# Optimization experiments

Measured on AMD Instinct MI355X. Metric: run time of the kernel, lower is better.

Reference implementation:

```python
import jax, jax.numpy as jnp
import numpy as np

B, C, DET, T = 16, 1, 512, 180  # batch, channels, detector size (= image side, circle=True), n angles


def setup_inputs() -> dict:
    key = jax.random.key(0)
    x = jax.random.normal(key, (B, C, DET, T), dtype=jnp.float32)  # sinogram [B,C,det,theta]
    return {"x": x}


def _ramp_filter(x):
    """skimage-style ramp (Ram-Lak) filter along detector axis (axis=2)."""
    det = x.shape[2]
    size = max(64, int(2 ** np.ceil(np.log2(2 * det))))  # zero-padded FFT length
    n = np.concatenate([np.arange(1, size // 2 + 1, 2), np.arange(size // 2 - 1, 0, -2)])
    f = np.zeros(size, dtype=np.float64)
    f[0] = 0.25
    f[1::2] = -1.0 / (np.pi * n) ** 2
    fourier = (2.0 * np.real(np.fft.fft(f))).astype(np.float32)  # [size]
    xp = jnp.pad(x, ((0, 0), (0, 0), (0, size - det), (0, 0)))
    proj = jnp.fft.fft(xp, axis=2) * fourier[None, None, :, None]
    return jnp.real(jnp.fft.ifft(proj, axis=2))[:, :, :det, :].astype(x.dtype)


def _forward(x):
    b, c, det, n_theta = x.shape
    xf = _ramp_filter(x)
    # align_corners=False unit grid over the image (circle=True -> grid side == det)
    u = ((2.0 * jnp.arange(det, dtype=x.dtype) + 1.0) / det - 1.0)
    yg = u[:, None]  # [det,1] (meshgrid 'ij': Y varies over rows)
    xg = u[None, :]  # [1,det]
    rad = jnp.arange(n_theta, dtype=x.dtype) * jnp.asarray(np.pi / 180.0, x.dtype)
    cos_t, sin_t = jnp.cos(rad), jnp.sin(rad)

    # Note: the grid X coord theta_x[i]=(2i+1)/T-1 maps (align_corners=False) to pixel
    # index exactly i, so the width-axis bilinear interp reduces to taking angle column i.
    def body(reco, inp):
        i, c_, s_ = inp
        col = jax.lax.dynamic_index_in_dim(xf, i, axis=3, keepdims=False)  # [B,C,det]
        t = xg * c_ - yg * s_                      # [det,det] rotated coordinate
        iy = ((t + 1.0) * det - 1.0) / 2.0         # grid_sample align_corners=False
        i0f = jnp.floor(iy)
        w1 = iy - i0f
        w0 = 1.0 - w1
        i0 = i0f.astype(jnp.int32)
        i1 = i0 + 1
        m0 = ((i0 >= 0) & (i0 < det)).astype(xf.dtype)  # zeros padding
        m1 = ((i1 >= 0) & (i1 < det)).astype(xf.dtype)
        g0 = jnp.take(col, jnp.clip(i0, 0, det - 1), axis=2)  # [B,C,det,det]
        g1 = jnp.take(col, jnp.clip(i1, 0, det - 1), axis=2)
        return reco + (w0 * m0) * g0 + (w1 * m1) * g1, None

    reco0 = jnp.zeros((b, c, det, det), xf.dtype)
    reco, _ = jax.lax.scan(body, reco0, (jnp.arange(n_theta), cos_t, sin_t))

    # reconstruction circle mask (scikit=False -> radius^2 <= 1 - 1/in_size)
    mask = (xg ** 2 + yg ** 2) <= (1.0 - 1.0 / det)
    reco = jnp.where(mask[None, None], reco, jnp.zeros((), reco.dtype))
    return reco * jnp.asarray(np.pi / (2.0 * n_theta), reco.dtype)


def reference(x):
    return _forward(x)
```

## Files before the change

kernel.cpp:

```cpp
#include <hip/hip_runtime.h>
#include <math.h>

#define DET 512
#define NB  16
#define NT  180
#define PI_D 3.14159265358979323846
#define NPAIR 89
#define PADQ 108
#define NGP  45
#define PKI_ROW 1536
#define NUNIT 113

#define TT_OFF   8192
#define XF0_OFF  (TT_OFF + 512*512*2)
#define XF90_OFF (XF0_OFF + 32768)
#define PK_OFF   (XF90_OFF + 32768)

typedef _Float16 half8  __attribute__((ext_vector_type(8)));
typedef _Float16 half4v __attribute__((ext_vector_type(4)));
typedef _Float16 half2v __attribute__((ext_vector_type(2)));
typedef float    float4v __attribute__((ext_vector_type(4)));

__device__ inline void fmix_lo(float& acc, float w, unsigned int pk) {
  asm("v_fma_mix_f32 %0, %1, %2, %0 op_sel_hi:[0,1,0]"
      : "+v"(acc) : "v"(w), "v"(pk));
}
__device__ inline void fmix_hi(float& acc, float w, unsigned int pk) {
  asm("v_fma_mix_f32 %0, %1, %2, %0 op_sel:[0,1,0] op_sel_hi:[0,1,0]"
      : "+v"(acc) : "v"(w), "v"(pk));
}

__global__ __launch_bounds__(256) void filter_kernel(const float* __restrict__ x,
                                                     char* __restrict__ wsb) {
  __shared__ _Float16 xs_h[16][512];
  __shared__ _Float16 xs_l[16][512];
  __shared__ float xfs[16][65];
  __shared__ _Float16 wls[8][1032];
  unsigned int* pkg = (unsigned int*)(wsb + PK_OFF);

  int tid = threadIdx.x;
  int p = blockIdx.x, b = blockIdx.y;
  int dt0 = blockIdx.z * 2;

  {
    int k0 = tid * 4;
    const float CSC = (float)(-2048.0 / (PI_D * PI_D));
#pragma unroll
    for (int r = 0; r < 8; r++) {
      half4v v;
#pragma unroll
      for (int j = 0; j < 4; j++) {
        int delta = 511 - (k0 + j) - r;
        float wv;
        if (delta == 0) wv = 512.0f;
        else if (delta & 1) wv = CSC / (float)(delta * delta);
        else wv = 0.0f;
        v[j] = (_Float16)wv;
      }
      *(half4v*)&wls[r][k0] = v;
    }
  }

  int m = tid & 15, kp = tid >> 4;
  int tS;
  if (p < 11) tS = (m < 8) ? (8 * p + 1 + m) : (164 - 8 * p + m);
  else        tS = (m == 0) ? 89 : ((m == 1) ? 91 : ((m == 3) ? 90 : 0));
  const float* xb = x + (size_t)b * DET * NT + tS;
#pragma unroll 8
  for (int pass = 0; pass < 16; pass++) {
    int k = pass * 32 + kp * 2;
    int c = k >> 3, h = k & 7;
    int phys = (((c ^ (m & 7)) << 3) | h);
    float v0 = xb[(size_t)k * NT];
    float v1 = xb[(size_t)(k + 1) * NT];
    _Float16 h0 = (_Float16)v0, h1 = (_Float16)v1;
    half2v hh = {h0, h1};
    half2v ll = {(_Float16)(v0 - (float)h0), (_Float16)(v1 - (float)h1)};
    *(half2v*)&xs_h[m][phys] = hh;
    *(half2v*)&xs_l[m][phys] = ll;
  }
  __syncthreads();

  int nprb = (p < 11) ? 8 : 1;
  int tpb0 = (p < 11) ? 8 * p : 88;
  if (blockIdx.z == 0) {
    int idx = (tid < 108) ? tid : (620 + (tid - 108));
    uint2 z2; z2.x = 0u; z2.y = 0u;
    for (int pr = 0; pr < nprb; pr++) {
      int tq = (p < 11) ? (tpb0 + pr) : 88;
      int gp = (tq <= 44) ? tq : 88 - tq;
      *(uint2*)&pkg[((size_t)b * NGP + gp) * PKI_ROW + 2 * idx] = z2;
    }
  }

  int lane = tid & 63, wv = tid >> 6;
  int mm = lane & 15, q = lane >> 4;
  const _Float16* arh = &xs_h[mm][0];
  const _Float16* arl = &xs_l[mm][0];
  int e = mm & 7;
  int mp = tid >> 5, cc = (tid & 31) * 2;
  int rT = (p < 11) ? mp : 0;
  int rU = (p < 11) ? (15 - mp) : 1;
  int tpp = (p < 11) ? (8 * p + mp) : 88;
  bool dopack = (p < 11) || (mp == 0);
  int gp_  = (tpp <= 44) ? tpp : 88 - tpp;
  int slot = (tpp <= 44) ? 0 : 1;

  for (int dti = 0; dti < 2; dti++) {
    int dt = dt0 + dti;
    int dw = dt * 64 + wv * 16 + mm;
    int sdw = 511 - dw;
    const _Float16* thl = &wls[sdw & 7][sdw & ~7];
    float4v acc0 = {0.f, 0.f, 0.f, 0.f};
    float4v acc1 = {0.f, 0.f, 0.f, 0.f};
#pragma unroll 4
    for (int kc = 0; kc < 512; kc += 32) {
      int ph = ((((kc >> 3) + q) ^ e) << 3);
      half8 Ah = *(const half8*)&arh[ph];
      half8 Al = *(const half8*)&arl[ph];
      half8 Bh = *(const half8*)&thl[kc + q * 8];
      acc0 = __builtin_amdgcn_mfma_f32_16x16x32_f16(Ah, Bh, acc0, 0, 0, 0);
      acc1 = __builtin_amdgcn_mfma_f32_16x16x32_f16(Al, Bh, acc1, 0, 0, 0);
    }
    if (dti > 0) __syncthreads();
#pragma unroll
    for (int i = 0; i < 4; i++)
      xfs[q * 4 + i][wv * 16 + mm] = (acc0[i] + acc1[i]) * 0.0009765625f;
    __syncthreads();
    if (dopack) {
      float ft0 = xfs[rT][cc], ft1 = xfs[rT][cc + 1];
      float fu0 = xfs[rU][cc], fu1 = xfs[rU][cc + 1];
      auto p0 = __builtin_amdgcn_cvt_pkrtz(ft0, fu0);
      auto p1 = __builtin_amdgcn_cvt_pkrtz(ft1, fu1);
      unsigned int w0, w1;
      __builtin_memcpy(&w0, &p0, 4);
      __builtin_memcpy(&w1, &p1, 4);
      unsigned int* row = pkg + ((size_t)b * NGP + gp_) * PKI_ROW;
      int en = PADQ + dt * 64 + cc;
      row[2 * en + slot]     = w0;
      row[2 * en + 2 + slot] = w1;
      if (tpp == 44) {
        row[2 * en + 1] = w0;
        row[2 * en + 3] = w1;
      }
    }
    if (p == 11 && tid < 64) {
      float* f0  = (float*)(wsb + XF0_OFF)  + (size_t)b * DET;
      float* f90 = (float*)(wsb + XF90_OFF) + (size_t)b * DET;
      f0[dt * 64 + tid]  = xfs[2][tid];
      f90[dt * 64 + tid] = xfs[3][tid];
    }
  }
}

#define PROCESS(c_, s_, SW)                                                    \
  {                                                                            \
    float inner = fmaf(-(s_), q_, 363.5f);                                     \
    float iyA = fmaf( (c_), p_, inner);                                        \
    float iyB = fmaf(-(c_), p_, inner);                                        \
    int   iA = (int)iyA;  float wA = __builtin_amdgcn_fractf(iyA);             \
    int   iB = (int)iyB;  float wB = __builtin_amdgcn_fractf(iyB);             \
    float vA = 1.f - wA, vB = 1.f - wB;                                        \
    uint4 rA, rB, rMA, rMB;                                                    \
    __builtin_memcpy(&rA,  &colI[2 * iA], 16);                                 \
    __builtin_memcpy(&rB,  &colI[2 * iB], 16);                                 \
    __builtin_memcpy(&rMA, &colI[2 * (726 - iA)], 16);                         \
    __builtin_memcpy(&rMB, &colI[2 * (726 - iB)], 16);                         \
    unsigned tA0 = SW ? rA.y : rA.x,  tA1 = SW ? rA.w : rA.z;                  \
    unsigned uA0 = SW ? rA.x : rA.y,  uA1 = SW ? rA.z : rA.w;                  \
    unsigned tB0 = SW ? rB.y : rB.x,  tB1 = SW ? rB.w : rB.z;                  \
    unsigned uB0 = SW ? rB.x : rB.y,  uB1 = SW ? rB.z : rB.w;                  \
    unsigned tMA0 = SW ? rMA.y : rMA.x,  tMA1 = SW ? rMA.w : rMA.z;            \
    unsigned uMA0 = SW ? rMA.x : rMA.y,  uMA1 = SW ? rMA.z : rMA.w;            \
    unsigned tMB0 = SW ? rMB.y : rMB.x,  tMB1 = SW ? rMB.w : rMB.z;            \
    unsigned uMB0 = SW ? rMB.x : rMB.y,  uMB1 = SW ? rMB.z : rMB.w;            \
    fmix_lo(A1, vA, tA0);  fmix_lo(A1, wA, tA1);                               \
    fmix_hi(A1, vB, tB0);  fmix_hi(A1, wB, tB1);                               \
    fmix_lo(A2, vB, tB0);  fmix_lo(A2, wB, tB1);                               \
    fmix_hi(A2, vA, tA0);  fmix_hi(A2, wA, tA1);                               \
    fmix_lo(A3, wA, tMA0); fmix_lo(A3, vA, tMA1);                              \
    fmix_hi(A3, wB, tMB0); fmix_hi(A3, vB, tMB1);                              \
    fmix_lo(A4, wB, tMB0); fmix_lo(A4, vB, tMB1);                              \
    fmix_hi(A4, wA, tMA0); fmix_hi(A4, vA, tMA1);                              \
    if (doQ) {                                                                 \
      fmix_lo(B1, wA, uMA0); fmix_lo(B1, vA, uMA1);                            \
      fmix_hi(B1, vB, uB0);  fmix_hi(B1, wB, uB1);                             \
      fmix_lo(B2, wB, uMB0); fmix_lo(B2, vB, uMB1);                            \
      fmix_hi(B2, vA, uA0);  fmix_hi(B2, wA, uA1);                             \
      fmix_lo(B3, vA, uA0);  fmix_lo(B3, wA, uA1);                             \
      fmix_hi(B3, wB, uMB0); fmix_hi(B3, vB, uMB1);                            \
      fmix_lo(B4, vB, uB0);  fmix_lo(B4, wB, uB1);                             \
      fmix_hi(B4, wA, uMA0); fmix_hi(B4, vA, uMA1);                            \
    }                                                                          \
  }

__global__ __launch_bounds__(256, 8) void backproj_kernel(
    const char* __restrict__ wsb, float* __restrict__ out) {
  __shared__ unsigned int pk[2][PKI_ROW];
  __shared__ float2 trigs[48];
  int tid = threadIdx.x;
  int b   = blockIdx.y;
  int bx  = blockIdx.x;
  int lx = tid & 15, ly = tid >> 4;
  float* ob = out + (size_t)b * DET * DET;

  if (bx == NUNIT) {
    const int LDEAD[10] = {10,8,6,5,4,3,2,2,1,1};
    for (int a = 0; a < 10; a++)
      for (int bt = 0; bt < LDEAD[a]; bt++) {
        int X1 = 16*a + lx, X2 = 511 - X1;
        int Y1 = 16*bt + ly, Y2 = 511 - Y1;
        ob[(size_t)Y1*DET + X1] = 0.f;
        ob[(size_t)Y1*DET + X2] = 0.f;
        ob[(size_t)Y2*DET + X1] = 0.f;
        ob[(size_t)Y2*DET + X2] = 0.f;
      }
    return;
  }

  int a = (bx>=6)+(bx>=14)+(bx>=24)+(bx>=35)+(bx>=47)+(bx>=58)+(bx>=68)
        + (bx>=77)+(bx>=85)+(bx>=92)+(bx>=98)+(bx>=103)+(bx>=107)+(bx>=110)+(bx>=112);
  int Sa, bs;
  if (a < 8) { Sa = (int)((0x443A2F23180E0600ULL >> (8*a)) & 0xFF);
               bs = (int)((0x070605040506080AULL >> (8*a)) & 0xFF); }
  else       { Sa = (int)((0x706E6B67625C554DULL >> (8*(a-8))) & 0xFF);
               bs = (int)((0x0F0E0D0C0B0A0908ULL >> (8*(a-8))) & 0xFF); }
  int bt = bx - Sa + bs;
  bool doQ = (a != bt);
  int tx = 16*a, ty = 16*bt;

  int X1 = tx + lx, X2 = 511 - X1;
  int Y1 = ty + ly, Y2 = 511 - Y1;
  float p_ = (float)X1 - 255.5f;
  float q_ = (float)Y1 - 255.5f;

  int w = tid >> 6, l = tid & 63;
  int mkx = 481 - 32*a;
  int mky = 505 - 32*bt - 8*w;
  bool wlive = (mkx*mkx + mky*mky <= 261632);

  if (tid < NGP) {
    float th = (float)(tid + 1) * (float)(PI_D / 180.0);
    float2 cs; cs.x = cosf(th); cs.y = sinf(th);
    trigs[tid] = cs;
  }

  const unsigned int* pkg = (const unsigned int*)(wsb + PK_OFF) + (size_t)b * NGP * PKI_ROW;

  float A1=0.f, A2=0.f, A3=0.f, A4=0.f;
  float B1=0.f, B2=0.f, B3=0.f, B4=0.f;

  auto stage_group = [&](int g, int par) {
    {
      const unsigned int* src = pkg + (size_t)g * PKI_ROW + w * 256 + l * 4;
      char* dst = (char*)&pk[par][0] + w * 1024;
      __builtin_amdgcn_global_load_lds(
          (const __attribute__((address_space(1))) unsigned int*)src,
          (__attribute__((address_space(3))) unsigned int*)dst, 16, 0, 0);
    }
    if (w < 2) {
      const unsigned int* src = pkg + (size_t)g * PKI_ROW + (w + 4) * 256 + l * 4;
      char* dst = (char*)&pk[par][0] + (w + 4) * 1024;
      __builtin_amdgcn_global_load_lds(
          (const __attribute__((address_space(1))) unsigned int*)src,
          (__attribute__((address_space(3))) unsigned int*)dst, 16, 0, 0);
    }
  };

  stage_group(0, 0);
  __syncthreads();

  for (int g = 0; g < NGP; g++) {
    if (g + 1 < NGP) stage_group(g + 1, (g + 1) & 1);
    float2 cs = trigs[g];
    const unsigned int* colI = &pk[g & 1][0];
    if (wlive) {
      PROCESS(cs.x, cs.y, 0);
      if (g != 44) PROCESS(cs.y, cs.x, 1);
    }
    __syncthreads();
  }

  const float* f0  = (const float*)(wsb + XF0_OFF)  + (size_t)b * DET;
  const float* f90 = (const float*)(wsb + XF90_OFF) + (size_t)b * DET;
  const float SC = (float)(PI_D / 360.0);
  int kx = 2*X1 - 511, ky = 2*Y1 - 511;
  bool in = (kx*kx + ky*ky) <= 261632;

  float g0x1 = f0[X1], g0x2 = f0[X2];
  float g90y1 = f90[Y1], g90y2 = f90[Y2];
  float P1 = A1 + g0x1 + g90y2;
  float P2 = A2 + g0x2 + g90y2;
  float P3 = A3 + g0x2 + g90y1;
  float P4 = A4 + g0x1 + g90y1;
  ob[(size_t)Y1*DET + X1] = in ? P1*SC : 0.f;
  ob[(size_t)Y1*DET + X2] = in ? P2*SC : 0.f;
  ob[(size_t)Y2*DET + X2] = in ? P3*SC : 0.f;
  ob[(size_t)Y2*DET + X1] = in ? P4*SC : 0.f;

  if (doQ) {
    float g0y1 = f0[Y1], g0y2 = f0[Y2];
    float g90x1 = f90[X1], g90x2 = f90[X2];
    float Q1 = B1 + g0y1 + g90x2;
    float Q2 = B2 + g0y1 + g90x1;
    float Q3 = B3 + g0y2 + g90x1;
    float Q4 = B4 + g0y2 + g90x2;
    Q1 = in ? Q1*SC : 0.f;
    Q2 = in ? Q2*SC : 0.f;
    Q3 = in ? Q3*SC : 0.f;
    Q4 = in ? Q4*SC : 0.f;
    __syncthreads();
    float* qs = (float*)&pk[0][0];
    qs[(0*16 + lx)*17 + ly] = Q1;
    qs[(1*16 + lx)*17 + ly] = Q2;
    qs[(2*16 + lx)*17 + ly] = Q3;
    qs[(3*16 + lx)*17 + ly] = Q4;
    __syncthreads();
    float o1 = qs[(0*16 + ly)*17 + lx];
    float o2 = qs[(1*16 + ly)*17 + lx];
    float o3 = qs[(2*16 + ly)*17 + lx];
    float o4 = qs[(3*16 + ly)*17 + lx];
    int r1 = tx + ly, r2 = 511 - r1;
    int c1 = ty + lx, c2 = 511 - c1;
    ob[(size_t)r1*DET + c1] = o1;
    ob[(size_t)r2*DET + c1] = o2;
    ob[(size_t)r2*DET + c2] = o3;
    ob[(size_t)r1*DET + c2] = o4;
  }
}

extern "C" void kernel_launch(void* const* d_in, const int* in_sizes, int n_in,
                              void* d_out, int out_size, void* d_ws, size_t ws_size,
                              hipStream_t stream) {
  (void)in_sizes; (void)n_in; (void)out_size; (void)ws_size;
  const float* x = (const float*)d_in[0];
  float* out = (float*)d_out;
  char*  wsb = (char*)d_ws;

  filter_kernel<<<dim3(12, 16, 4), 256, 0, stream>>>(x, wsb);
  backproj_kernel<<<dim3(NUNIT + 1, 16), 256, 0, stream>>>(wsb, out);
}
```

Before: 142.1 us.

## Process two batch images per backprojection block to share coordinate math

Each backprojection block now handles two batch items. The per-pixel interpolation coordinates and weights are computed once and reused for both images' LDS columns. LDS staging, accumulators and output writes are doubled, the grid's batch dimension is halved, and launch bounds drop to 4 blocks/SM. This amortizes the index/weight arithmetic and trig setup, at the cost of more registers and LDS per block, fewer blocks (less parallelism), and lower occupancy.

```diff
diff --git a/kernel.cpp b/kernel.cpp
--- a/kernel.cpp
+++ b/kernel.cpp
@@ -153,6 +153,41 @@
   }
 }
 
+#define RDFMIX(colX, rr, SW)                                                   \
+  {                                                                            \
+    uint4 rA, rB, rMA, rMB;                                                    \
+    __builtin_memcpy(&rA,  &colX[2 * iA], 16);                                 \
+    __builtin_memcpy(&rB,  &colX[2 * iB], 16);                                 \
+    __builtin_memcpy(&rMA, &colX[2 * (726 - iA)], 16);                         \
+    __builtin_memcpy(&rMB, &colX[2 * (726 - iB)], 16);                         \
+    unsigned tA0 = SW ? rA.y : rA.x,  tA1 = SW ? rA.w : rA.z;                  \
+    unsigned uA0 = SW ? rA.x : rA.y,  uA1 = SW ? rA.z : rA.w;                  \
+    unsigned tB0 = SW ? rB.y : rB.x,  tB1 = SW ? rB.w : rB.z;                  \
+    unsigned uB0 = SW ? rB.x : rB.y,  uB1 = SW ? rB.z : rB.w;                  \
+    unsigned tMA0 = SW ? rMA.y : rMA.x,  tMA1 = SW ? rMA.w : rMA.z;            \
+    unsigned uMA0 = SW ? rMA.x : rMA.y,  uMA1 = SW ? rMA.z : rMA.w;            \
+    unsigned tMB0 = SW ? rMB.y : rMB.x,  tMB1 = SW ? rMB.w : rMB.z;            \
+    unsigned uMB0 = SW ? rMB.x : rMB.y,  uMB1 = SW ? rMB.z : rMB.w;            \
+    fmix_lo(A1[rr], vA, tA0);  fmix_lo(A1[rr], wA, tA1);                       \
+    fmix_hi(A1[rr], vB, tB0);  fmix_hi(A1[rr], wB, tB1);                       \
+    fmix_lo(A2[rr], vB, tB0);  fmix_lo(A2[rr], wB, tB1);                       \
+    fmix_hi(A2[rr], vA, tA0);  fmix_hi(A2[rr], wA, tA1);                       \
+    fmix_lo(A3[rr], wA, tMA0); fmix_lo(A3[rr], vA, tMA1);                      \
+    fmix_hi(A3[rr], wB, tMB0); fmix_hi(A3[rr], vB, tMB1);                      \
+    fmix_lo(A4[rr], wB, tMB0); fmix_lo(A4[rr], vB, tMB1);                      \
+    fmix_hi(A4[rr], wA, tMA0); fmix_hi(A4[rr], vA, tMA1);                      \
+    if (doQ) {                                                                 \
+      fmix_lo(B1[rr], wA, uMA0); fmix_lo(B1[rr], vA, uMA1);                    \
+      fmix_hi(B1[rr], vB, uB0);  fmix_hi(B1[rr], wB, uB1);                     \
+      fmix_lo(B2[rr], wB, uMB0); fmix_lo(B2[rr], vB, uMB1);                    \
+      fmix_hi(B2[rr], vA, uA0);  fmix_hi(B2[rr], wA, uA1);                     \
+      fmix_lo(B3[rr], vA, uA0);  fmix_lo(B3[rr], wA, uA1);                     \
+      fmix_hi(B3[rr], wB, uMB0); fmix_hi(B3[rr], vB, uMB1);                    \
+      fmix_lo(B4[rr], vB, uB0);  fmix_lo(B4[rr], wB, uB1);                     \
+      fmix_hi(B4[rr], wA, uMA0); fmix_hi(B4[rr], vA, uMA1);                    \
+    }                                                                          \
+  }
+
 #define PROCESS(c_, s_, SW)                                                    \
   {                                                                            \
     float inner = fmaf(-(s_), q_, 363.5f);                                     \
@@ -161,48 +196,20 @@
     int   iA = (int)iyA;  float wA = __builtin_amdgcn_fractf(iyA);             \
     int   iB = (int)iyB;  float wB = __builtin_amdgcn_fractf(iyB);             \
     float vA = 1.f - wA, vB = 1.f - wB;                                        \
-    uint4 rA, rB, rMA, rMB;                                                    \
-    __builtin_memcpy(&rA,  &colI[2 * iA], 16);                                 \
-    __builtin_memcpy(&rB,  &colI[2 * iB], 16);                                 \
-    __builtin_memcpy(&rMA, &colI[2 * (726 - iA)], 16);                         \
-    __builtin_memcpy(&rMB, &colI[2 * (726 - iB)], 16);                         \
-    unsigned tA0 = SW ? rA.y : rA.x,  tA1 = SW ? rA.w : rA.z;                  \
-    unsigned uA0 = SW ? rA.x : rA.y,  uA1 = SW ? rA.z : rA.w;                  \
-    unsigned tB0 = SW ? rB.y : rB.x,  tB1 = SW ? rB.w : rB.z;                  \
-    unsigned uB0 = SW ? rB.x : rB.y,  uB1 = SW ? rB.z : rB.w;                  \
-    unsigned tMA0 = SW ? rMA.y : rMA.x,  tMA1 = SW ? rMA.w : rMA.z;            \
-    unsigned uMA0 = SW ? rMA.x : rMA.y,  uMA1 = SW ? rMA.z : rMA.w;            \
-    unsigned tMB0 = SW ? rMB.y : rMB.x,  tMB1 = SW ? rMB.w : rMB.z;            \
-    unsigned uMB0 = SW ? rMB.x : rMB.y,  uMB1 = SW ? rMB.z : rMB.w;            \
-    fmix_lo(A1, vA, tA0);  fmix_lo(A1, wA, tA1);                               \
-    fmix_hi(A1, vB, tB0);  fmix_hi(A1, wB, tB1);                               \
-    fmix_lo(A2, vB, tB0);  fmix_lo(A2, wB, tB1);                               \
-    fmix_hi(A2, vA, tA0);  fmix_hi(A2, wA, tA1);                               \
-    fmix_lo(A3, wA, tMA0); fmix_lo(A3, vA, tMA1);                              \
-    fmix_hi(A3, wB, tMB0); fmix_hi(A3, vB, tMB1);                              \
-    fmix_lo(A4, wB, tMB0); fmix_lo(A4, vB, tMB1);                              \
-    fmix_hi(A4, wA, tMA0); fmix_hi(A4, vA, tMA1);                              \
-    if (doQ) {                                                                 \
-      fmix_lo(B1, wA, uMA0); fmix_lo(B1, vA, uMA1);                            \
-      fmix_hi(B1, vB, uB0);  fmix_hi(B1, wB, uB1);                             \
-      fmix_lo(B2, wB, uMB0); fmix_lo(B2, vB, uMB1);                            \
-      fmix_hi(B2, vA, uA0);  fmix_hi(B2, wA, uA1);                             \
-      fmix_lo(B3, vA, uA0);  fmix_lo(B3, wA, uA1);                             \
-      fmix_hi(B3, wB, uMB0); fmix_hi(B3, vB, uMB1);                            \
-      fmix_lo(B4, vB, uB0);  fmix_lo(B4, wB, uB1);                             \
-      fmix_hi(B4, wA, uMA0); fmix_hi(B4, vA, uMA1);                            \
-    }                                                                          \
-  }
-
-__global__ __launch_bounds__(256, 8) void backproj_kernel(
+    RDFMIX(colI0, 0, SW)                                                       \
+    RDFMIX(colI1, 1, SW)                                                       \
+  }
+
+__global__ __launch_bounds__(256, 4) void backproj_kernel(
     const char* __restrict__ wsb, float* __restrict__ out) {
-  __shared__ unsigned int pk[2][PKI_ROW];
+  __shared__ unsigned int pk[2][2][PKI_ROW];
   __shared__ float2 trigs[48];
   int tid = threadIdx.x;
-  int b   = blockIdx.y;
+  int b0  = blockIdx.y * 2;
   int bx  = blockIdx.x;
   int lx = tid & 15, ly = tid >> 4;
-  float* ob = out + (size_t)b * DET * DET;
+  float* ob0 = out + (size_t)b0 * DET * DET;
+  float* ob1 = out + (size_t)(b0 + 1) * DET * DET;
 
   if (bx == NUNIT) {
     const int LDEAD[10] = {10,8,6,5,4,3,2,2,1,1};
@@ -210,10 +217,10 @@
       for (int bt = 0; bt < LDEAD[a]; bt++) {
         int X1 = 16*a + lx, X2 = 511 - X1;
         int Y1 = 16*bt + ly, Y2 = 511 - Y1;
-        ob[(size_t)Y1*DET + X1] = 0.f;
-        ob[(size_t)Y1*DET + X2] = 0.f;
-        ob[(size_t)Y2*DET + X1] = 0.f;
-        ob[(size_t)Y2*DET + X2] = 0.f;
+        ob0[(size_t)Y1*DET + X1] = 0.f;  ob1[(size_t)Y1*DET + X1] = 0.f;
+        ob0[(size_t)Y1*DET + X2] = 0.f;  ob1[(size_t)Y1*DET + X2] = 0.f;
+        ob0[(size_t)Y2*DET + X1] = 0.f;  ob1[(size_t)Y2*DET + X1] = 0.f;
+        ob0[(size_t)Y2*DET + X2] = 0.f;  ob1[(size_t)Y2*DET + X2] = 0.f;
       }
     return;
   }
@@ -245,26 +252,24 @@
     trigs[tid] = cs;
   }
 
-  const unsigned int* pkg = (const unsigned int*)(wsb + PK_OFF) + (size_t)b * NGP * PKI_ROW;
-
-  float A1=0.f, A2=0.f, A3=0.f, A4=0.f;
-  float B1=0.f, B2=0.f, B3=0.f, B4=0.f;
+  const unsigned int* pkg0 = (const unsigned int*)(wsb + PK_OFF) + (size_t)b0 * NGP * PKI_ROW;
+  const unsigned int* pkg1 = pkg0 + (size_t)NGP * PKI_ROW;
+
+  float A1[2]={0,0}, A2[2]={0,0}, A3[2]={0,0}, A4[2]={0,0};
+  float B1[2]={0,0}, B2[2]={0,0}, B3[2]={0,0}, B4[2]={0,0};
 
   auto stage_group = [&](int g, int par) {
-    {
-      const unsigned int* src = pkg + (size_t)g * PKI_ROW + w * 256 + l * 4;
-      char* dst = (char*)&pk[par][0] + w * 1024;
+#pragma unroll
+    for (int i = 0; i < 3; i++) {
+      int c = w + 4 * i;
+      int r = (c < 6) ? 0 : 1;
+      int off = (c < 6) ? c : (c - 6);
+      const unsigned int* src = (r ? pkg1 : pkg0) + (size_t)g * PKI_ROW + off * 256 + l * 4;
+      char* dst = (char*)&pk[par][r][0] + off * 1024;
       __builtin_amdgcn_global_load_lds(
           (const __attribute__((address_space(1))) unsigned int*)src,
           (__attribute__((address_space(3))) unsigned int*)dst, 16, 0, 0);
     }
-    if (w < 2) {
-      const unsigned int* src = pkg + (size_t)g * PKI_ROW + (w + 4) * 256 + l * 4;
-      char* dst = (char*)&pk[par][0] + (w + 4) * 1024;
-      __builtin_amdgcn_global_load_lds(
-          (const __attribute__((address_space(1))) unsigned int*)src,
-          (__attribute__((address_space(3))) unsigned int*)dst, 16, 0, 0);
-    }
   };
 
   stage_group(0, 0);
@@ -273,7 +278,8 @@
   for (int g = 0; g < NGP; g++) {
     if (g + 1 < NGP) stage_group(g + 1, (g + 1) & 1);
     float2 cs = trigs[g];
-    const unsigned int* colI = &pk[g & 1][0];
+    const unsigned int* colI0 = &pk[g & 1][0][0];
+    const unsigned int* colI1 = &pk[g & 1][1][0];
     if (wlive) {
       PROCESS(cs.x, cs.y, 0);
       if (g != 44) PROCESS(cs.y, cs.x, 1);
@@ -281,51 +287,61 @@
     __syncthreads();
   }
 
-  const float* f0  = (const float*)(wsb + XF0_OFF)  + (size_t)b * DET;
-  const float* f90 = (const float*)(wsb + XF90_OFF) + (size_t)b * DET;
   const float SC = (float)(PI_D / 360.0);
   int kx = 2*X1 - 511, ky = 2*Y1 - 511;
   bool in = (kx*kx + ky*ky) <= 261632;
 
-  float g0x1 = f0[X1], g0x2 = f0[X2];
-  float g90y1 = f90[Y1], g90y2 = f90[Y2];
-  float P1 = A1 + g0x1 + g90y2;
-  float P2 = A2 + g0x2 + g90y2;
-  float P3 = A3 + g0x2 + g90y1;
-  float P4 = A4 + g0x1 + g90y1;
-  ob[(size_t)Y1*DET + X1] = in ? P1*SC : 0.f;
-  ob[(size_t)Y1*DET + X2] = in ? P2*SC : 0.f;
-  ob[(size_t)Y2*DET + X2] = in ? P3*SC : 0.f;
-  ob[(size_t)Y2*DET + X1] = in ? P4*SC : 0.f;
+  float Qs[2][4];
+#pragma unroll
+  for (int rr = 0; rr < 2; rr++) {
+    const float* f0  = (const float*)(wsb + XF0_OFF)  + (size_t)(b0 + rr) * DET;
+    const float* f90 = (const float*)(wsb + XF90_OFF) + (size_t)(b0 + rr) * DET;
+    float* ob = rr ? ob1 : ob0;
+    float g0x1 = f0[X1], g0x2 = f0[X2];
+    float g90y1 = f90[Y1], g90y2 = f90[Y2];
+    float P1 = A1[rr] + g0x1 + g90y2;
+    float P2 = A2[rr] + g0x2 + g90y2;
+    float P3 = A3[rr] + g0x2 + g90y1;
+    float P4 = A4[rr] + g0x1 + g90y1;
+    ob[(size_t)Y1*DET + X1] = in ? P1*SC : 0.f;
+    ob[(size_t)Y1*DET + X2] = in ? P2*SC : 0.f;
+    ob[(size_t)Y2*DET + X2] = in ? P3*SC : 0.f;
+    ob[(size_t)Y2*DET + X1] = in ? P4*SC : 0.f;
+    if (doQ) {
+      float g0y1 = f0[Y1], g0y2 = f0[Y2];
+      float g90x1 = f90[X1], g90x2 = f90[X2];
+      Qs[rr][0] = in ? (B1[rr] + g0y1 + g90x2) * SC : 0.f;
+      Qs[rr][1] = in ? (B2[rr] + g0y1 + g90x1) * SC : 0.f;
+      Qs[rr][2] = in ? (B3[rr] + g0y2 + g90x1) * SC : 0.f;
+      Qs[rr][3] = in ? (B4[rr] + g0y2 + g90x2) * SC : 0.f;
+    }
+  }
 
   if (doQ) {
-    float g0y1 = f0[Y1], g0y2 = f0[Y2];
-    float g90x1 = f90[X1], g90x2 = f90[X2];
-    float Q1 = B1 + g0y1 + g90x2;
-    float Q2 = B2 + g0y1 + g90x1;
-    float Q3 = B3 + g0y2 + g90x1;
-    float Q4 = B4 + g0y2 + g90x2;
-    Q1 = in ? Q1*SC : 0.f;
-    Q2 = in ? Q2*SC : 0.f;
-    Q3 = in ? Q3*SC : 0.f;
-    Q4 = in ? Q4*SC : 0.f;
     __syncthreads();
-    float* qs = (float*)&pk[0][0];
-    qs[(0*16 + lx)*17 + ly] = Q1;
-    qs[(1*16 + lx)*17 + ly] = Q2;
-    qs[(2*16 + lx)*17 + ly] = Q3;
-    qs[(3*16 + lx)*17 + ly] = Q4;
+    float* qs0 = (float*)&pk[0][0][0];
+    float* qs1 = (float*)&pk[0][1][0];
+#pragma unroll
+    for (int i = 0; i < 4; i++) {
+      qs0[(i*16 + lx)*17 + ly] = Qs[0][i];
+      qs1[(i*16 + lx)*17 + ly] = Qs[1][i];
+    }
     __syncthreads();
-    float o1 = qs[(0*16 + ly)*17 + lx];
-    float o2 = qs[(1*16 + ly)*17 + lx];
-    float o3 = qs[(2*16 + ly)*17 + lx];
-    float o4 = qs[(3*16 + ly)*17 + lx];
     int r1 = tx + ly, r2 = 511 - r1;
     int c1 = ty + lx, c2 = 511 - c1;
-    ob[(size_t)r1*DET + c1] = o1;
-    ob[(size_t)r2*DET + c1] = o2;
-    ob[(size_t)r2*DET + c2] = o3;
-    ob[(size_t)r1*DET + c2] = o4;
+#pragma unroll
+    for (int rr = 0; rr < 2; rr++) {
+      float* qs = rr ? qs1 : qs0;
+      float* ob = rr ? ob1 : ob0;
+      float o1 = qs[(0*16 + ly)*17 + lx];
+      float o2 = qs[(1*16 + ly)*17 + lx];
+      float o3 = qs[(2*16 + ly)*17 + lx];
+      float o4 = qs[(3*16 + ly)*17 + lx];
+      ob[(size_t)r1*DET + c1] = o1;
+      ob[(size_t)r2*DET + c1] = o2;
+      ob[(size_t)r2*DET + c2] = o3;
+      ob[(size_t)r1*DET + c2] = o4;
+    }
   }
 }
 
@@ -338,5 +354,5 @@
   char*  wsb = (char*)d_ws;
 
   filter_kernel<<<dim3(12, 16, 4), 256, 0, stream>>>(x, wsb);
-  backproj_kernel<<<dim3(NUNIT + 1, 16), 256, 0, stream>>>(wsb, out);
-}
+  backproj_kernel<<<dim3(NUNIT + 1, NB / 2), 256, 0, stream>>>(wsb, out);
+}
```

New measurement: 145.4 us. +2.4%, slower.

## Merge diagonal tile pairs into single blocks and drop doQ branch from off-diagonal path

Applied to the files above, without the earlier changes.

Diagonal tiles (a==bt), which only computed the P half of the symmetric work, are now paired two per block in a dedicated path that processes two diagonal tiles sharing the same staged LDS columns. Off-diagonal blocks always do the Q work, so the per-angle doQ branch disappears, and the grid shrinks from 114 to 108 blocks per batch. The aim is better load balance, since diagonal blocks no longer run half-empty, and fewer redundant staging passes. The cost is a more complex index mapping and a second specialised code path, which can raise register pressure.

```diff
diff --git a/kernel.cpp b/kernel.cpp
--- a/kernel.cpp
+++ b/kernel.cpp
@@ -9,7 +9,9 @@
 #define PADQ 108
 #define NGP  45
 #define PKI_ROW 1536
-#define NUNIT 113
+#define NOFF 101
+#define NMRG 6
+#define NBX  108
 
 #define TT_OFF   8192
 #define XF0_OFF  (TT_OFF + 512*512*2)
@@ -152,6 +154,7 @@
     }
   }
 }
+
 
 #define PROCESS(c_, s_, SW)                                                    \
   {                                                                            \
@@ -182,16 +185,41 @@
     fmix_hi(A3, wB, tMB0); fmix_hi(A3, vB, tMB1);                              \
     fmix_lo(A4, wB, tMB0); fmix_lo(A4, vB, tMB1);                              \
     fmix_hi(A4, wA, tMA0); fmix_hi(A4, vA, tMA1);                              \
-    if (doQ) {                                                                 \
-      fmix_lo(B1, wA, uMA0); fmix_lo(B1, vA, uMA1);                            \
-      fmix_hi(B1, vB, uB0);  fmix_hi(B1, wB, uB1);                             \
-      fmix_lo(B2, wB, uMB0); fmix_lo(B2, vB, uMB1);                            \
-      fmix_hi(B2, vA, uA0);  fmix_hi(B2, wA, uA1);                             \
-      fmix_lo(B3, vA, uA0);  fmix_lo(B3, wA, uA1);                             \
-      fmix_hi(B3, wB, uMB0); fmix_hi(B3, vB, uMB1);                            \
-      fmix_lo(B4, vB, uB0);  fmix_lo(B4, wB, uB1);                             \
-      fmix_hi(B4, wA, uMA0); fmix_hi(B4, vA, uMA1);                            \
-    }                                                                          \
+    fmix_lo(B1, wA, uMA0); fmix_lo(B1, vA, uMA1);                              \
+    fmix_hi(B1, vB, uB0);  fmix_hi(B1, wB, uB1);                               \
+    fmix_lo(B2, wB, uMB0); fmix_lo(B2, vB, uMB1);                              \
+    fmix_hi(B2, vA, uA0);  fmix_hi(B2, wA, uA1);                               \
+    fmix_lo(B3, vA, uA0);  fmix_lo(B3, wA, uA1);                               \
+    fmix_hi(B3, wB, uMB0); fmix_hi(B3, vB, uMB1);                              \
+    fmix_lo(B4, vB, uB0);  fmix_lo(B4, wB, uB1);                               \
+    fmix_hi(B4, wA, uMA0); fmix_hi(B4, vA, uMA1);                              \
+  }
+
+#define PROCESSP(c_, s_, SW, pp, qq, AA1, AA2, AA3, AA4)                       \
+  {                                                                            \
+    float inner = fmaf(-(s_), (qq), 363.5f);                                   \
+    float iyA = fmaf( (c_), (pp), inner);                                      \
+    float iyB = fmaf(-(c_), (pp), inner);                                      \
+    int   iA = (int)iyA;  float wA = __builtin_amdgcn_fractf(iyA);             \
+    int   iB = (int)iyB;  float wB = __builtin_amdgcn_fractf(iyB);             \
+    float vA = 1.f - wA, vB = 1.f - wB;                                        \
+    uint4 rA, rB, rMA, rMB;                                                    \
+    __builtin_memcpy(&rA,  &colI[2 * iA], 16);                                 \
+    __builtin_memcpy(&rB,  &colI[2 * iB], 16);                                 \
+    __builtin_memcpy(&rMA, &colI[2 * (726 - iA)], 16);                         \
+    __builtin_memcpy(&rMB, &colI[2 * (726 - iB)], 16);                         \
+    unsigned tA0 = SW ? rA.y : rA.x,  tA1 = SW ? rA.w : rA.z;                  \
+    unsigned tB0 = SW ? rB.y : rB.x,  tB1 = SW ? rB.w : rB.z;                  \
+    unsigned tMA0 = SW ? rMA.y : rMA.x,  tMA1 = SW ? rMA.w : rMA.z;            \
+    unsigned tMB0 = SW ? rMB.y : rMB.x,  tMB1 = SW ? rMB.w : rMB.z;            \
+    fmix_lo(AA1, vA, tA0);  fmix_lo(AA1, wA, tA1);                             \
+    fmix_hi(AA1, vB, tB0);  fmix_hi(AA1, wB, tB1);                             \
+    fmix_lo(AA2, vB, tB0);  fmix_lo(AA2, wB, tB1);                             \
+    fmix_hi(AA2, vA, tA0);  fmix_hi(AA2, wA, tA1);                             \
+    fmix_lo(AA3, wA, tMA0); fmix_lo(AA3, vA, tMA1);                            \
+    fmix_hi(AA3, wB, tMB0); fmix_hi(AA3, vB, tMB1);                            \
+    fmix_lo(AA4, wB, tMB0); fmix_lo(AA4, vB, tMB1);                            \
+    fmix_hi(AA4, wA, tMA0); fmix_hi(AA4, vA, tMA1);                            \
   }
 
 __global__ __launch_bounds__(256, 8) void backproj_kernel(
@@ -203,8 +231,9 @@
   int bx  = blockIdx.x;
   int lx = tid & 15, ly = tid >> 4;
   float* ob = out + (size_t)b * DET * DET;
-
-  if (bx == NUNIT) {
+  int w = tid >> 6, l = tid & 63;
+
+  if (bx == NOFF + NMRG) {
     const int LDEAD[10] = {10,8,6,5,4,3,2,2,1,1};
     for (int a = 0; a < 10; a++)
       for (int bt = 0; bt < LDEAD[a]; bt++) {
@@ -218,27 +247,6 @@
     return;
   }
 
-  int a = (bx>=6)+(bx>=14)+(bx>=24)+(bx>=35)+(bx>=47)+(bx>=58)+(bx>=68)
-        + (bx>=77)+(bx>=85)+(bx>=92)+(bx>=98)+(bx>=103)+(bx>=107)+(bx>=110)+(bx>=112);
-  int Sa, bs;
-  if (a < 8) { Sa = (int)((0x443A2F23180E0600ULL >> (8*a)) & 0xFF);
-               bs = (int)((0x070605040506080AULL >> (8*a)) & 0xFF); }
-  else       { Sa = (int)((0x706E6B67625C554DULL >> (8*(a-8))) & 0xFF);
-               bs = (int)((0x0F0E0D0C0B0A0908ULL >> (8*(a-8))) & 0xFF); }
-  int bt = bx - Sa + bs;
-  bool doQ = (a != bt);
-  int tx = 16*a, ty = 16*bt;
-
-  int X1 = tx + lx, X2 = 511 - X1;
-  int Y1 = ty + ly, Y2 = 511 - Y1;
-  float p_ = (float)X1 - 255.5f;
-  float q_ = (float)Y1 - 255.5f;
-
-  int w = tid >> 6, l = tid & 63;
-  int mkx = 481 - 32*a;
-  int mky = 505 - 32*bt - 8*w;
-  bool wlive = (mkx*mkx + mky*mky <= 261632);
-
   if (tid < NGP) {
     float th = (float)(tid + 1) * (float)(PI_D / 180.0);
     float2 cs; cs.x = cosf(th); cs.y = sinf(th);
@@ -246,9 +254,6 @@
   }
 
   const unsigned int* pkg = (const unsigned int*)(wsb + PK_OFF) + (size_t)b * NGP * PKI_ROW;
-
-  float A1=0.f, A2=0.f, A3=0.f, A4=0.f;
-  float B1=0.f, B2=0.f, B3=0.f, B4=0.f;
 
   auto stage_group = [&](int g, int par) {
     {
@@ -267,6 +272,82 @@
     }
   };
 
+  const float* f0  = (const float*)(wsb + XF0_OFF)  + (size_t)b * DET;
+  const float* f90 = (const float*)(wsb + XF90_OFF) + (size_t)b * DET;
+  const float SC = (float)(PI_D / 360.0);
+
+  if (bx >= NOFF) {
+    int d = bx - NOFF;
+    int a1 = 4 + 2 * d, a2 = 5 + 2 * d;
+    float p1_ = (float)(16 * a1 + lx) - 255.5f, q1_ = (float)(16 * a1 + ly) - 255.5f;
+    float p2_ = (float)(16 * a2 + lx) - 255.5f, q2_ = (float)(16 * a2 + ly) - 255.5f;
+    int mk1 = 481 - 32 * a1, mn1 = 505 - 32 * a1 - 8 * w;
+    int mk2 = 481 - 32 * a2, mn2 = 505 - 32 * a2 - 8 * w;
+    bool wl1 = (mk1 * mk1 + mn1 * mn1 <= 261632);
+    bool wl2 = (mk2 * mk2 + mn2 * mn2 <= 261632);
+
+    float A1=0.f, A2=0.f, A3=0.f, A4=0.f;
+    float C1=0.f, C2=0.f, C3=0.f, C4=0.f;
+
+    stage_group(0, 0);
+    __syncthreads();
+    for (int g = 0; g < NGP; g++) {
+      if (g + 1 < NGP) stage_group(g + 1, (g + 1) & 1);
+      float2 cs = trigs[g];
+      const unsigned int* colI = &pk[g & 1][0];
+      if (wl1) {
+        PROCESSP(cs.x, cs.y, 0, p1_, q1_, A1, A2, A3, A4);
+        if (g != 44) PROCESSP(cs.y, cs.x, 1, p1_, q1_, A1, A2, A3, A4);
+      }
+      if (wl2) {
+        PROCESSP(cs.x, cs.y, 0, p2_, q2_, C1, C2, C3, C4);
+        if (g != 44) PROCESSP(cs.y, cs.x, 1, p2_, q2_, C1, C2, C3, C4);
+      }
+      __syncthreads();
+    }
+#pragma unroll
+    for (int t = 0; t < 2; t++) {
+      int a = t ? a2 : a1;
+      int X1 = 16 * a + lx, X2 = 511 - X1;
+      int Y1 = 16 * a + ly, Y2 = 511 - Y1;
+      int kx = 2 * X1 - 511, ky = 2 * Y1 - 511;
+      bool in = (kx * kx + ky * ky) <= 261632;
+      float g0x1 = f0[X1], g0x2 = f0[X2];
+      float g90y1 = f90[Y1], g90y2 = f90[Y2];
+      float P1 = (t ? C1 : A1) + g0x1 + g90y2;
+      float P2 = (t ? C2 : A2) + g0x2 + g90y2;
+      float P3 = (t ? C3 : A3) + g0x2 + g90y1;
+      float P4 = (t ? C4 : A4) + g0x1 + g90y1;
+      ob[(size_t)Y1 * DET + X1] = in ? P1 * SC : 0.f;
+      ob[(size_t)Y1 * DET + X2] = in ? P2 * SC : 0.f;
+      ob[(size_t)Y2 * DET + X2] = in ? P3 * SC : 0.f;
+      ob[(size_t)Y2 * DET + X1] = in ? P4 * SC : 0.f;
+    }
+    return;
+  }
+
+  int a = (bx>=6)+(bx>=14)+(bx>=24)+(bx>=35)+(bx>=46)+(bx>=56)+(bx>=65)
+        + (bx>=73)+(bx>=80)+(bx>=86)+(bx>=91)+(bx>=95)+(bx>=98)+(bx>=100);
+  int Sa, bs;
+  if (a < 8) { Sa = (int)((0x41382E23180E0600ULL >> (8*a)) & 0xFF);
+               bs = (int)((0x080706050506080AULL >> (8*a)) & 0xFF); }
+  else       { Sa = (int)((0x0064625F5B565049ULL >> (8*(a-8))) & 0xFF);
+               bs = (int)((0x000F0E0D0C0B0A09ULL >> (8*(a-8))) & 0xFF); }
+  int bt = bx - Sa + bs;
+  int tx = 16*a, ty = 16*bt;
+
+  int X1 = tx + lx, X2 = 511 - X1;
+  int Y1 = ty + ly, Y2 = 511 - Y1;
+  float p_ = (float)X1 - 255.5f;
+  float q_ = (float)Y1 - 255.5f;
+
+  int mkx = 481 - 32*a;
+  int mky = 505 - 32*bt - 8*w;
+  bool wlive = (mkx*mkx + mky*mky <= 261632);
+
+  float A1=0.f, A2=0.f, A3=0.f, A4=0.f;
+  float B1=0.f, B2=0.f, B3=0.f, B4=0.f;
+
   stage_group(0, 0);
   __syncthreads();
 
@@ -281,9 +362,6 @@
     __syncthreads();
   }
 
-  const float* f0  = (const float*)(wsb + XF0_OFF)  + (size_t)b * DET;
-  const float* f90 = (const float*)(wsb + XF90_OFF) + (size_t)b * DET;
-  const float SC = (float)(PI_D / 360.0);
   int kx = 2*X1 - 511, ky = 2*Y1 - 511;
   bool in = (kx*kx + ky*ky) <= 261632;
 
@@ -298,7 +376,7 @@
   ob[(size_t)Y2*DET + X2] = in ? P3*SC : 0.f;
   ob[(size_t)Y2*DET + X1] = in ? P4*SC : 0.f;
 
-  if (doQ) {
+  {
     float g0y1 = f0[Y1], g0y2 = f0[Y2];
     float g90x1 = f90[X1], g90x2 = f90[X2];
     float Q1 = B1 + g0y1 + g90x2;
@@ -338,5 +416,5 @@
   char*  wsb = (char*)d_ws;
 
   filter_kernel<<<dim3(12, 16, 4), 256, 0, stream>>>(x, wsb);
-  backproj_kernel<<<dim3(NUNIT + 1, 16), 256, 0, stream>>>(wsb, out);
+  backproj_kernel<<<dim3(NBX, NB), 256, 0, stream>>>(wsb, out);
 }
```

After: 139.2 us. -2.0%, faster.
